# Kernel tuning notes

Measured on AMD Instinct MI355X. Metric: run time of the kernel, lower is better.

The kernel has to match this reference:

```python
import jax, jax.numpy as jnp
import numpy as np

B, S, D = 2, 2048, 1024
H, HD = 16, 64          # n_heads, head_dim (H*HD == D)
E, K, F = 8, 2, 1024    # n_experts, top_k, expert hidden size
EPS = 1e-6


def setup_inputs() -> dict:
    key = jax.random.key(0)
    ks = jax.random.split(key, 10)
    g = lambda k, shape, sc: jax.random.normal(k, shape, jnp.float32) * sc
    return {
        "x": g(ks[0], (B, S, D), 1.0),
        "attn_norm_w": jnp.ones((D,), jnp.float32),
        "wq": g(ks[1], (D, D), 0.02),
        "wk": g(ks[2], (D, D), 0.02),
        "wv": g(ks[3], (D, D), 0.02),
        "wo": g(ks[4], (D, D), 0.02),
        "ffn_norm_w": jnp.ones((D,), jnp.float32),
        "router_w": g(ks[5], (D, E), 0.02),
        "w1": g(ks[6], (E, D, F), 0.02),  # gate proj per expert
        "w3": g(ks[7], (E, D, F), 0.02),  # up proj per expert
        "w2": g(ks[8], (E, F, D), 0.02),  # down proj per expert
    }


def rmsnorm(x, w):
    return x * jax.lax.rsqrt(jnp.mean(x * x, axis=-1, keepdims=True) + EPS) * w


def attention(x, wq, wk, wv, wo):
    b, s, d = x.shape
    q = (x @ wq).reshape(b, s, H, HD)
    k = (x @ wk).reshape(b, s, H, HD)
    v = (x @ wv).reshape(b, s, H, HD)
    scores = jnp.einsum("bqhd,bkhd->bhqk", q, k) / jnp.sqrt(jnp.float32(HD))
    causal = jnp.tril(jnp.ones((s, s), bool))
    scores = jnp.where(causal, scores, jnp.finfo(scores.dtype).min)
    p = jax.nn.softmax(scores, axis=-1)
    o = jnp.einsum("bhqk,bkhd->bqhd", p, v).reshape(b, s, d)
    return o @ wo


def moe_ffn(x, router_w, w1, w2, w3):
    b, s, d = x.shape
    xt = x.reshape(-1, d)                       # [T, D]
    probs = jax.nn.softmax(xt @ router_w, axis=-1)  # [T, E]
    gate, idx = jax.lax.top_k(probs, K)         # [T, K]
    gate = gate / jnp.sum(gate, axis=-1, keepdims=True)  # renormalize top-k
    T = xt.shape[0]
    combine = jnp.zeros((T, E), xt.dtype).at[jnp.arange(T)[:, None], idx].set(gate)
    out = jnp.zeros_like(xt)
    for e in range(E):  # fixed small loop over experts (dense-equivalent dispatch)
        h = jax.nn.silu(xt @ w1[e]) * (xt @ w3[e])
        out = out + combine[:, e:e + 1] * (h @ w2[e])
    return out.reshape(b, s, d)


def reference(x, attn_norm_w, wq, wk, wv, wo, ffn_norm_w, router_w, w1, w2, w3):
    # h = x + dropout(attn(norm(x)));  out = h + dropout(moe(norm(h)))  (dropout=0)
    h = x + attention(rmsnorm(x, attn_norm_w), wq, wk, wv, wo)
    return h + moe_ffn(rmsnorm(h, ffn_norm_w), router_w, w1, w2, w3)
```

## Files before the change

### kernel.cpp

```cpp
#include <hip/hip_runtime.h>
#include <cstdint>
#include <math.h>

typedef unsigned short u16;
typedef unsigned int u32;
typedef __bf16 bf16x8 __attribute__((ext_vector_type(8)));
typedef float f32x4 __attribute__((ext_vector_type(4)));

#define TBATCH 2
#define TSEQ   2048
#define TDIM   1024
#define THEADS 16
#define THDIM  64
#define TEXP   8
#define TFF    1024
#define TTOK   (TBATCH*TSEQ)
#define TPAIRS (TTOK*2)

__device__ __forceinline__ u16 f2bf(float f) {
  u32 u = __float_as_uint(f);
  u += 0x7FFFu + ((u >> 16) & 1u);
  return (u16)(u >> 16);
}
__device__ __forceinline__ u16 f2bft(float f) {
  return (u16)(__float_as_uint(f) >> 16);
}
__device__ __forceinline__ float bf2f(u16 h) { return __uint_as_float(((u32)h) << 16); }
__device__ __forceinline__ float fexp2(float x) {
  float r;
  asm("v_exp_f32 %0, %1" : "=v"(r) : "v"(x));
  return r;
}

__device__ __forceinline__ void gll16(const void* g, void* l) {
  __builtin_amdgcn_global_load_lds((const __attribute__((address_space(1))) void*)g,
                                   (__attribute__((address_space(3))) void*)l, 16, 0, 0);
}
__device__ __forceinline__ bf16x8 ldsread(const void* p) { return *(const bf16x8*)p; }
__device__ __forceinline__ f32x4 mm16(bf16x8 a, bf16x8 b, f32x4 c) {
  return __builtin_amdgcn_mfma_f32_16x16x32_bf16(a, b, c, 0, 0, 0);
}
__device__ __forceinline__ f32x4 fzero() { f32x4 z = {0.f, 0.f, 0.f, 0.f}; return z; }

__global__ void transpose_all_k(const float* __restrict__ wq, const float* __restrict__ wk,
                                const float* __restrict__ wv, const float* __restrict__ wo,
                                const float* __restrict__ w1, const float* __restrict__ w3,
                                const float* __restrict__ w2,
                                u16* __restrict__ qth, u16* __restrict__ qtl,
                                u16* __restrict__ kth, u16* __restrict__ ktl,
                                u16* __restrict__ vth_, u16* __restrict__ vtl_,
                                u16* __restrict__ oth, u16* __restrict__ otl,
                                u16* __restrict__ w1t, u16* __restrict__ w3t, u16* __restrict__ w2t) {
  __shared__ float t[32][33];
  int id = (int)blockIdx.x;
  const float* in; u16* outh; u16* outl = nullptr;
  size_t bo = 0;
  int tile;
  if (id < 4096) {
    const int wi = id >> 10;
    in   = (wi == 0) ? wq  : (wi == 1) ? wk  : (wi == 2) ? wv   : wo;
    outh = (wi == 0) ? qth : (wi == 1) ? kth : (wi == 2) ? vth_ : oth;
    outl = (wi == 0) ? qtl : (wi == 1) ? ktl : (wi == 2) ? vtl_ : otl;
    tile = id & 1023;
  } else {
    const int id2 = id - 4096;
    const int wi = id2 >> 13;
    const int rem = id2 & 8191;
    bo = (size_t)(rem >> 10) << 20;
    in   = (wi == 0) ? w1  : (wi == 1) ? w3  : w2;
    outh = (wi == 0) ? w1t : (wi == 1) ? w3t : w2t;
    tile = rem & 1023;
  }
  const int c0 = (tile & 31) * 32, r0 = (tile >> 5) * 32;
  const int tx = threadIdx.x, ty = threadIdx.y;
#pragma unroll
  for (int j = 0; j < 32; j += 8)
    t[ty + j][tx] = in[bo + (size_t)(r0 + ty + j) * 1024 + (c0 + tx)];
  __syncthreads();
#pragma unroll
  for (int j = 0; j < 32; j += 8) {
    float v = t[tx][ty + j];
    u16 hv = f2bf(v);
    size_t o = bo + (size_t)(c0 + ty + j) * 1024 + (r0 + tx);
    outh[o] = hv;
    if (outl != nullptr) outl[o] = f2bf(v - bf2f(hv));
  }
}

__launch_bounds__(256)
__global__ void rmsnorm_k(const float* __restrict__ x, const float* __restrict__ w,
                          u16* __restrict__ oh, u16* __restrict__ ol) {
  const int t = blockIdx.x, tid = threadIdx.x;
  const float4 xv = ((const float4*)(x + (size_t)t * TDIM))[tid];
  float ss = xv.x*xv.x + xv.y*xv.y + xv.z*xv.z + xv.w*xv.w;
#pragma unroll
  for (int d = 1; d < 64; d <<= 1) ss += __shfl_xor(ss, d, 64);
  __shared__ float sp[4];
  if ((tid & 63) == 0) sp[tid >> 6] = ss;
  __syncthreads();
  const float rsc = rsqrtf((sp[0] + sp[1] + sp[2] + sp[3]) * (1.0f / TDIM) + 1e-6f);
  const float4 wv = ((const float4*)w)[tid];
  float v0 = xv.x*rsc*wv.x, v1 = xv.y*rsc*wv.y, v2 = xv.z*rsc*wv.z, v3 = xv.w*rsc*wv.w;
  u16 h0 = f2bf(v0), h1 = f2bf(v1), h2 = f2bf(v2), h3 = f2bf(v3);
  uint2 ph; ph.x = (u32)h0 | ((u32)h1 << 16); ph.y = (u32)h2 | ((u32)h3 << 16);
  *(uint2*)(oh + (size_t)t * TDIM + tid * 4) = ph;
  u16 l0 = f2bf(v0 - bf2f(h0)), l1 = f2bf(v1 - bf2f(h1));
  u16 l2 = f2bf(v2 - bf2f(h2)), l3 = f2bf(v3 - bf2f(h3));
  uint2 pl; pl.x = (u32)l0 | ((u32)l1 << 16); pl.y = (u32)l2 | ((u32)l3 << 16);
  *(uint2*)(ol + (size_t)t * TDIM + tid * 4) = pl;
}

__launch_bounds__(256)
__global__ void gemm_qkv_k(const u16* __restrict__ Ah, const u16* __restrict__ Al,
                           const u16* __restrict__ Bqh, const u16* __restrict__ Bql,
                           const u16* __restrict__ Bkh, const u16* __restrict__ Bkl,
                           const u16* __restrict__ Bvh, const u16* __restrict__ Bvl,
                           u16* __restrict__ qh, u16* __restrict__ ql,
                           u16* __restrict__ kh, u16* __restrict__ kl,
                           u16* __restrict__ vth, u16* __restrict__ vtl) {
  __shared__ u16 sAh[2][128 * 32], sAl[2][128 * 32], sBh[2][64 * 32], sBl[2][64 * 32];
  const int tid = threadIdx.x, wid = tid >> 6, lane = tid & 63;
  const int which = blockIdx.y >> 4;
  const int m0 = blockIdx.x * 128, n0 = (blockIdx.y & 15) * 64;
  const int wr = wid >> 1, wc = wid & 1;
  const u16* Bth = (which == 0) ? Bqh : (which == 1) ? Bkh : Bvh;
  const u16* Btl = (which == 0) ? Bql : (which == 1) ? Bkl : Bvl;
  u16* outh = (which == 0) ? qh : kh;
  u16* outl = (which == 0) ? ql : kl;

  f32x4 acc[4][2];
#pragma unroll
  for (int i = 0; i < 4; i++)
#pragma unroll
    for (int j = 0; j < 2; j++) acc[i][j] = fzero();

  const int srow = tid >> 2;
  const int scol = (((tid & 3) ^ ((tid >> 3) & 3)) * 8);
  const size_t a0 = (size_t)(m0 + srow) * TDIM + scol;
  const size_t a1 = (size_t)(m0 + srow + 64) * TDIM + scol;
  const size_t b0 = (size_t)(n0 + srow) * TDIM + scol;
  const int ldsw = wid * 1024;

  const int g = (lane >> 1) & 3;
  int aoffs[4], boffs[2];
#pragma unroll
  for (int mf = 0; mf < 4; mf++)
    aoffs[mf] = (wr*64 + mf*16 + (lane & 15)) * 64 + ((((lane >> 4)) ^ g) << 4);
#pragma unroll
  for (int nf = 0; nf < 2; nf++)
    boffs[nf] = (wc*32 + nf*16 + (lane & 15)) * 64 + ((((lane >> 4)) ^ g) << 4);

  auto stage = [&](int kk, int bi) {
    const int ke = kk * 32;
    gll16(Ah + a0 + ke, (char*)sAh[bi] + ldsw);
    gll16(Ah + a1 + ke, (char*)sAh[bi] + 4096 + ldsw);
    gll16(Al + a0 + ke, (char*)sAl[bi] + ldsw);
    gll16(Al + a1 + ke, (char*)sAl[bi] + 4096 + ldsw);
    gll16(Bth + b0 + ke, (char*)sBh[bi] + ldsw);
    gll16(Btl + b0 + ke, (char*)sBl[bi] + ldsw);
  };

  stage(0, 0);
  asm volatile("s_waitcnt vmcnt(0)" ::: "memory");
  __builtin_amdgcn_s_barrier();

  for (int kk = 0; kk < 32; ++kk) {
    const int cur = kk & 1;
    if (kk + 1 < 32) stage(kk + 1, cur ^ 1);
    bf16x8 fah[4], fal[4], fbh[2], fbl[2];
#pragma unroll
    for (int mf = 0; mf < 4; mf++) { fah[mf] = ldsread((char*)sAh[cur] + aoffs[mf]); fal[mf] = ldsread((char*)sAl[cur] + aoffs[mf]); }
#pragma unroll
    for (int nf = 0; nf < 2; nf++) { fbh[nf] = ldsread((char*)sBh[cur] + boffs[nf]); fbl[nf] = ldsread((char*)sBl[cur] + boffs[nf]); }
#pragma unroll
    for (int mf = 0; mf < 4; mf++)
#pragma unroll
      for (int nf = 0; nf < 2; nf++) {
        acc[mf][nf] = mm16(fah[mf], fbh[nf], acc[mf][nf]);
        acc[mf][nf] = mm16(fah[mf], fbl[nf], acc[mf][nf]);
        acc[mf][nf] = mm16(fal[mf], fbh[nf], acc[mf][nf]);
      }
    asm volatile("s_waitcnt vmcnt(0)" ::: "memory");
    __builtin_amdgcn_s_barrier();
  }

#pragma unroll
  for (int mf = 0; mf < 4; mf++)
#pragma unroll
    for (int nf = 0; nf < 2; nf++)
#pragma unroll
      for (int r = 0; r < 4; r++) {
        const int grow = m0 + wr*64 + mf*16 + ((lane >> 4) * 4) + r;
        const int gcol = n0 + wc*32 + nf*16 + (lane & 15);
        const float v = acc[mf][nf][r];
        u16 hv = f2bf(v);
        u16 lv = f2bf(v - bf2f(hv));
        if (which < 2) {
          const size_t o = (size_t)grow * TDIM + gcol;
          outh[o] = hv; outl[o] = lv;
        } else {
          const int b = grow >> 11, s = grow & (TSEQ - 1);
          const int hh = gcol >> 6, hd = gcol & 63;
          const size_t o = ((size_t)((b * THEADS + hh) * THDIM + hd)) * TSEQ + s;
          vth[o] = hv; vtl[o] = lv;
        }
      }
}

template<int EPI>
__launch_bounds__(256)
__global__ void gemm_x3_k(const u16* __restrict__ Ah, const u16* __restrict__ Al,
                          const u16* __restrict__ Bth, const u16* __restrict__ Btl,
                          u16* __restrict__ outh, u16* __restrict__ outl,
                          float* __restrict__ outf, const float* __restrict__ resid,
                          int M, int N, int K) {
  __shared__ u16 sAh[2][128 * 32], sAl[2][128 * 32], sBh[2][64 * 32], sBl[2][64 * 32];
  const int tid = threadIdx.x, wid = tid >> 6, lane = tid & 63;
  const int m0 = blockIdx.x * 128, n0 = blockIdx.y * 64;
  const int wr = wid >> 1, wc = wid & 1;

  f32x4 acc[4][2];
#pragma unroll
  for (int i = 0; i < 4; i++)
#pragma unroll
    for (int j = 0; j < 2; j++) acc[i][j] = fzero();

  const int srow = tid >> 2;
  const int scol = (((tid & 3) ^ ((tid >> 3) & 3)) * 8);
  const size_t a0 = (size_t)(m0 + srow) * K + scol;
  const size_t a1 = (size_t)(m0 + srow + 64) * K + scol;
  const size_t b0 = (size_t)(n0 + srow) * K + scol;
  const int ldsw = wid * 1024;

  const int g = (lane >> 1) & 3;
  int aoffs[4], boffs[2];
#pragma unroll
  for (int mf = 0; mf < 4; mf++)
    aoffs[mf] = (wr*64 + mf*16 + (lane & 15)) * 64 + ((((lane >> 4)) ^ g) << 4);
#pragma unroll
  for (int nf = 0; nf < 2; nf++)
    boffs[nf] = (wc*32 + nf*16 + (lane & 15)) * 64 + ((((lane >> 4)) ^ g) << 4);

  auto stage = [&](int kk, int bi) {
    const int ke = kk * 32;
    gll16(Ah + a0 + ke, (char*)sAh[bi] + ldsw);
    gll16(Ah + a1 + ke, (char*)sAh[bi] + 4096 + ldsw);
    gll16(Al + a0 + ke, (char*)sAl[bi] + ldsw);
    gll16(Al + a1 + ke, (char*)sAl[bi] + 4096 + ldsw);
    gll16(Bth + b0 + ke, (char*)sBh[bi] + ldsw);
    gll16(Btl + b0 + ke, (char*)sBl[bi] + ldsw);
  };

  const int nk = K >> 5;
  stage(0, 0);
  asm volatile("s_waitcnt vmcnt(0)" ::: "memory");
  __builtin_amdgcn_s_barrier();

  for (int kk = 0; kk < nk; ++kk) {
    const int cur = kk & 1;
    if (kk + 1 < nk) stage(kk + 1, cur ^ 1);
    bf16x8 fah[4], fal[4], fbh[2], fbl[2];
#pragma unroll
    for (int mf = 0; mf < 4; mf++) { fah[mf] = ldsread((char*)sAh[cur] + aoffs[mf]); fal[mf] = ldsread((char*)sAl[cur] + aoffs[mf]); }
#pragma unroll
    for (int nf = 0; nf < 2; nf++) { fbh[nf] = ldsread((char*)sBh[cur] + boffs[nf]); fbl[nf] = ldsread((char*)sBl[cur] + boffs[nf]); }
#pragma unroll
    for (int mf = 0; mf < 4; mf++)
#pragma unroll
      for (int nf = 0; nf < 2; nf++) {
        acc[mf][nf] = mm16(fah[mf], fbh[nf], acc[mf][nf]);
        acc[mf][nf] = mm16(fah[mf], fbl[nf], acc[mf][nf]);
        acc[mf][nf] = mm16(fal[mf], fbh[nf], acc[mf][nf]);
      }
    asm volatile("s_waitcnt vmcnt(0)" ::: "memory");
    __builtin_amdgcn_s_barrier();
  }

#pragma unroll
  for (int mf = 0; mf < 4; mf++)
#pragma unroll
    for (int nf = 0; nf < 2; nf++)
#pragma unroll
      for (int r = 0; r < 4; r++) {
        const int grow = m0 + wr*64 + mf*16 + ((lane >> 4) * 4) + r;
        const int gcol = n0 + wc*32 + nf*16 + (lane & 15);
        const float v = acc[mf][nf][r];
        if (EPI == 0) {
          const size_t o = (size_t)grow * N + gcol;
          u16 hv = f2bf(v);
          outh[o] = hv; outl[o] = f2bf(v - bf2f(hv));
        } else if (EPI == 1) {
          const int b = grow >> 11, s = grow & (TSEQ - 1);
          const int hh = gcol >> 6, hd = gcol & 63;
          const size_t o = ((size_t)((b * THEADS + hh) * THDIM + hd)) * TSEQ + s;
          u16 hv = f2bf(v);
          outh[o] = hv; outl[o] = f2bf(v - bf2f(hv));
        } else {
          const size_t o = (size_t)grow * N + gcol;
          outf[o] = v + resid[o];
        }
      }
}

__launch_bounds__(256, 3)
__global__ void flash_k(const u16* __restrict__ Qh, const u16* __restrict__ Ql,
                        const u16* __restrict__ Kh, const u16* __restrict__ Kl,
                        const u16* __restrict__ Vth, const u16* __restrict__ Vtl,
                        u16* __restrict__ Oh, u16* __restrict__ Ol) {
  __shared__ u16 sK[2][2][2048];
  __shared__ u16 sV[2][2][2048];
  __shared__ u16 sP[2][4][512];
  const int tid = threadIdx.x, wid = tid >> 6, lane = tid & 63;
  const int qb = (int)(gridDim.x - 1 - blockIdx.x);
  const int bh = blockIdx.y;
  const int b = bh >> 4, h = bh & 15;
  const float SCL = 0.125f * 1.4426950408889634f;

  bf16x8 fqh[2][2], fql[2][2];
#pragma unroll
  for (int hh = 0; hh < 2; hh++) {
    const size_t qbase = ((size_t)(b * TSEQ + qb * 128 + hh * 64 + wid * 16 + (lane & 15))) * TDIM + h * 64;
#pragma unroll
    for (int kq = 0; kq < 2; kq++) {
      fqh[hh][kq] = *(const bf16x8*)(Qh + qbase + (kq * 4 + (lane >> 4)) * 8);
      fql[hh][kq] = *(const bf16x8*)(Ql + qbase + (kq * 4 + (lane >> 4)) * 8);
    }
  }

  f32x4 oacc[2][4];
  float m_run[2][4], l_lane[2][4];
#pragma unroll
  for (int hh = 0; hh < 2; hh++)
#pragma unroll
    for (int i = 0; i < 4; i++) { oacc[hh][i] = fzero(); m_run[hh][i] = -INFINITY; l_lane[hh][i] = 0.f; }

  const int ksrow = tid >> 3;
  const int ksxcol = (((lane & 7) ^ ((lane >> 3) & 7)) << 3);
  const size_t kg0 = ((size_t)(b * TSEQ + ksrow)) * TDIM + h * 64 + ksxcol;
  const int vsrow = tid >> 2;
  const int vsxcol = (((tid & 3) ^ ((tid >> 3) & 3)) << 3);
  const size_t vg0 = ((size_t)((b * THEADS + h) * THDIM + vsrow)) * TSEQ + vsxcol;

  auto stage = [&](int kb, int bi) {
    const size_t ko = (size_t)kb * 32 * TDIM;
    const size_t vo = (size_t)kb * 32;
    const int wofs = wid * 1024;
    gll16(Kh + kg0 + ko, (char*)sK[bi][0] + wofs);
    gll16(Kl + kg0 + ko, (char*)sK[bi][1] + wofs);
    gll16(Vth + vg0 + vo, (char*)sV[bi][0] + wofs);
    gll16(Vtl + vg0 + vo, (char*)sV[bi][1] + wofs);
  };

  const int nkb = 4 * qb + 4;
  stage(0, 0);
  asm volatile("s_waitcnt vmcnt(0)" ::: "memory");
  __builtin_amdgcn_s_barrier();

  for (int kb = 0; kb < nkb; ++kb) {
    const int cur = kb & 1;
    if (kb + 1 < nkb) stage(kb + 1, cur ^ 1);

    const bool act0 = (kb * 32 <= qb * 128 + 63);

    f32x4 sc[2][2];
#pragma unroll
    for (int nf = 0; nf < 2; nf++) {
      f32x4 s0 = fzero(), s1 = fzero();
      const int krow = nf * 16 + (lane & 15);
#pragma unroll
      for (int kq = 0; kq < 2; kq++) {
        const int off = krow * 128 + (((kq * 4 + (lane >> 4)) ^ (lane & 7)) << 4);
        bf16x8 kfh = ldsread((char*)sK[cur][0] + off);
        bf16x8 kfl = ldsread((char*)sK[cur][1] + off);
        s0 = mm16(fqh[0][kq], kfh, s0);
        s0 = mm16(fqh[0][kq], kfl, s0);
        s0 = mm16(fql[0][kq], kfh, s0);
        s1 = mm16(fqh[1][kq], kfh, s1);
        s1 = mm16(fqh[1][kq], kfl, s1);
        s1 = mm16(fql[1][kq], kfh, s1);
      }
      sc[0][nf] = s0; sc[1][nf] = s1;
    }

    bf16x8 pa_h[2], pa_l[2];
#pragma unroll
    for (int hh = 0; hh < 2; hh++) {
      if (hh == 0 && !act0) continue;

      const int qg = qb * 128 + hh * 64 + wid * 16 + ((lane >> 4) * 4);
      float pm[4] = {-INFINITY, -INFINITY, -INFINITY, -INFINITY};
#pragma unroll
      for (int nf = 0; nf < 2; nf++) {
        const int kg = kb * 32 + nf * 16 + (lane & 15);
#pragma unroll
        for (int r = 0; r < 4; r++) {
          float v = sc[hh][nf][r] * SCL;
          if (kg > qg + r) v = -INFINITY;
          sc[hh][nf][r] = v;
          pm[r] = fmaxf(pm[r], v);
        }
      }
#pragma unroll
      for (int r = 0; r < 4; r++)
#pragma unroll
        for (int d = 1; d < 16; d <<= 1) pm[r] = fmaxf(pm[r], __shfl_xor(pm[r], d, 64));

      float mn[4], esc[4];
#pragma unroll
      for (int r = 0; r < 4; r++) {
        mn[r] = fmaxf(m_run[hh][r], pm[r]);
        esc[r] = fexp2(m_run[hh][r] - mn[r]);
        m_run[hh][r] = mn[r];
      }
      float ls[4] = {0.f, 0.f, 0.f, 0.f};
#pragma unroll
      for (int nf = 0; nf < 2; nf++)
#pragma unroll
        for (int r = 0; r < 4; r++) {
          float p = fexp2(sc[hh][nf][r] - mn[r]);
          sc[hh][nf][r] = p;
          ls[r] += p;
        }
#pragma unroll
      for (int r = 0; r < 4; r++) l_lane[hh][r] = l_lane[hh][r] * esc[r] + ls[r];
#pragma unroll
      for (int nf = 0; nf < 4; nf++)
#pragma unroll
        for (int r = 0; r < 4; r++) oacc[hh][nf][r] *= esc[r];

#pragma unroll
      for (int nf = 0; nf < 2; nf++)
#pragma unroll
        for (int r = 0; r < 4; r++) {
          float p = sc[hh][nf][r];
          u16 ph = f2bft(p);
          const int prow = (lane >> 4) * 4 + r;
          const int pbyte = (prow * 64 + (nf * 16 + (lane & 15)) * 2) ^ (((prow >> 1) & 3) << 4);
          *(u16*)((char*)sP[0][wid] + pbyte) = ph;
          *(u16*)((char*)sP[1][wid] + pbyte) = f2bft(p - bf2f(ph));
        }

      {
        const int prow = lane & 15;
        const int poff = (prow * 64 + ((lane >> 4) << 4)) ^ ((((prow >> 1) & 3)) << 4);
        pa_h[hh] = ldsread((char*)sP[0][wid] + poff);
        pa_l[hh] = ldsread((char*)sP[1][wid] + poff);
      }
    }

#pragma unroll
    for (int nf = 0; nf < 4; nf++) {
      const int vrow = nf * 16 + (lane & 15);
      const int voff = vrow * 64 + ((((lane >> 4) ^ ((lane >> 1) & 3)) & 3) << 4);
      bf16x8 vfh = ldsread((char*)sV[cur][0] + voff);
      bf16x8 vfl = ldsread((char*)sV[cur][1] + voff);
      if (act0) {
        oacc[0][nf] = mm16(pa_h[0], vfh, oacc[0][nf]);
        oacc[0][nf] = mm16(pa_h[0], vfl, oacc[0][nf]);
        oacc[0][nf] = mm16(pa_l[0], vfh, oacc[0][nf]);
      }
      oacc[1][nf] = mm16(pa_h[1], vfh, oacc[1][nf]);
      oacc[1][nf] = mm16(pa_h[1], vfl, oacc[1][nf]);
      oacc[1][nf] = mm16(pa_l[1], vfh, oacc[1][nf]);
    }

    asm volatile("s_waitcnt vmcnt(0)" ::: "memory");
    __builtin_amdgcn_s_barrier();
  }

#pragma unroll
  for (int hh = 0; hh < 2; hh++)
#pragma unroll
    for (int r = 0; r < 4; r++) {
      float lt = l_lane[hh][r];
#pragma unroll
      for (int d = 1; d < 16; d <<= 1) lt += __shfl_xor(lt, d, 64);
      const float inv = 1.0f / lt;
      const int t = b * TSEQ + qb * 128 + hh * 64 + wid * 16 + ((lane >> 4) * 4) + r;
#pragma unroll
      for (int nf = 0; nf < 4; nf++) {
        const float v = oacc[hh][nf][r] * inv;
        const size_t o = (size_t)t * TDIM + h * 64 + nf * 16 + (lane & 15);
        u16 hv = f2bft(v);
        Oh[o] = hv; Ol[o] = f2bft(v - bf2f(hv));
      }
    }
}

__launch_bounds__(256)
__global__ void router_k(const float* __restrict__ hres, const float* __restrict__ wn,
                         const float* __restrict__ rw, u16* __restrict__ hn,
                         int* __restrict__ idx01, float* __restrict__ gate01,
                         int* __restrict__ counts) {
  const int t = blockIdx.x, tid = threadIdx.x;
  const float4 xv = ((const float4*)(hres + (size_t)t * TDIM))[tid];
  float ss = xv.x*xv.x + xv.y*xv.y + xv.z*xv.z + xv.w*xv.w;
#pragma unroll
  for (int d = 1; d < 64; d <<= 1) ss += __shfl_xor(ss, d, 64);
  __shared__ float sp[4];
  __shared__ float sacc[4][8];
  if ((tid & 63) == 0) sp[tid >> 6] = ss;
  __syncthreads();
  const float rsc = rsqrtf((sp[0]+sp[1]+sp[2]+sp[3]) * (1.0f / TDIM) + 1e-6f);
  const float4 wv = ((const float4*)wn)[tid];
  const float x0 = xv.x*rsc*wv.x, x1 = xv.y*rsc*wv.y, x2 = xv.z*rsc*wv.z, x3 = xv.w*rsc*wv.w;
  {
    u16 h0 = f2bf(x0), h1 = f2bf(x1), h2 = f2bf(x2), h3 = f2bf(x3);
    uint2 ph; ph.x = (u32)h0 | ((u32)h1 << 16); ph.y = (u32)h2 | ((u32)h3 << 16);
    *(uint2*)(hn + (size_t)t * TDIM + tid * 4) = ph;
  }
  const float* rp = rw + (size_t)(tid * 4) * TEXP;
  float acc[8];
#pragma unroll
  for (int e = 0; e < 8; e++) acc[e] = x0*rp[e] + x1*rp[8+e] + x2*rp[16+e] + x3*rp[24+e];
#pragma unroll
  for (int e = 0; e < 8; e++)
#pragma unroll
    for (int d = 1; d < 64; d <<= 1) acc[e] += __shfl_xor(acc[e], d, 64);
  if ((tid & 63) == 0)
#pragma unroll
    for (int e = 0; e < 8; e++) sacc[tid >> 6][e] = acc[e];
  __syncthreads();
  if (tid == 0) {
    float lg[8];
#pragma unroll
    for (int e = 0; e < 8; e++) lg[e] = sacc[0][e] + sacc[1][e] + sacc[2][e] + sacc[3][e];
    int i1 = 0;
#pragma unroll
    for (int e = 1; e < 8; e++) if (lg[e] > lg[i1]) i1 = e;
    int i2 = (i1 == 0) ? 1 : 0;
#pragma unroll
    for (int e = 0; e < 8; e++) if (e != i1 && lg[e] > lg[i2]) i2 = e;
    const float g1 = 1.0f / (1.0f + __expf(lg[i2] - lg[i1]));
    idx01[t*2] = i1; idx01[t*2+1] = i2;
    gate01[t*2] = g1; gate01[t*2+1] = 1.0f - g1;
    atomicAdd(&counts[i1], 1);
    atomicAdd(&counts[i2], 1);
  }
}

__global__ void zero8_k(int* counts) { if (threadIdx.x < TEXP) counts[threadIdx.x] = 0; }

__global__ void offsets_k(const int* __restrict__ counts, int* __restrict__ cursor,
                          int* __restrict__ bm_e, int* __restrict__ bm_s0,
                          int* __restrict__ bm_end, int* __restrict__ n_active) {
  if (threadIdx.x != 0 || blockIdx.x != 0) return;
  int off = 0, nb = 0;
  for (int e = 0; e < TEXP; e++) {
    const int c = counts[e];
    cursor[e] = off;
    const int end = off + c;
    for (int mb = 0; mb * 128 < c; mb++) { bm_e[nb] = e; bm_s0[nb] = off + mb * 128; bm_end[nb] = end; nb++; }
    off = end;
  }
  *n_active = nb;
}

__global__ void scatter_k(const int* __restrict__ idx01, int* __restrict__ cursor,
                          int* __restrict__ slot_of, int* __restrict__ perm) {
  const int t = blockIdx.x * 256 + threadIdx.x;
  if (t >= TTOK) return;
#pragma unroll
  for (int k = 0; k < 2; k++) {
    const int e = idx01[t*2+k];
    const int slot = atomicAdd(&cursor[e], 1);
    slot_of[t*2+k] = slot;
    perm[slot] = t;
  }
}

__launch_bounds__(256)
__global__ void moe_gemm1_k(const u16* __restrict__ hn, const u16* __restrict__ w1t,
                            const u16* __restrict__ w3t, const int* __restrict__ perm,
                            const int* __restrict__ bm_e, const int* __restrict__ bm_s0,
                            const int* __restrict__ bm_end, const int* __restrict__ n_active,
                            u16* __restrict__ hbuf) {
  if ((int)blockIdx.x >= *n_active) return;
  __shared__ u16 sA[2][128 * 32], sB1[2][64 * 32], sB3[2][64 * 32];
  const int tid = threadIdx.x, wid = tid >> 6, lane = tid & 63;
  const int e = bm_e[blockIdx.x], slot0 = bm_s0[blockIdx.x], send = bm_end[blockIdx.x];
  const int n0 = blockIdx.y * 64;
  const int wr = wid >> 1, wc = wid & 1;
  const int srow = tid >> 2;
  const int scol = (((tid & 3) ^ ((tid >> 3) & 3)) * 8);
  const int sa0 = slot0 + srow, sa1 = slot0 + srow + 64;
  const int ta = (sa0 < send) ? perm[sa0] : 0;
  const int tb2 = (sa1 < send) ? perm[sa1] : 0;
  const size_t a0 = (size_t)ta * TDIM + scol;
  const size_t a1 = (size_t)tb2 * TDIM + scol;
  const size_t bb = (size_t)e * TDIM * TFF + (size_t)(n0 + srow) * TDIM + scol;
  const int ldsw = wid * 1024;
  f32x4 ac1[4][2], ac3[4][2];
#pragma unroll
  for (int i = 0; i < 4; i++)
#pragma unroll
    for (int j = 0; j < 2; j++) { ac1[i][j] = fzero(); ac3[i][j] = fzero(); }
  const int g = (lane >> 1) & 3;
  int aoffs[4], boffs[2];
#pragma unroll
  for (int mf = 0; mf < 4; mf++)
    aoffs[mf] = (wr*64 + mf*16 + (lane & 15)) * 64 + ((((lane >> 4)) ^ g) << 4);
#pragma unroll
  for (int nf = 0; nf < 2; nf++)
    boffs[nf] = (wc*32 + nf*16 + (lane & 15)) * 64 + ((((lane >> 4)) ^ g) << 4);

  auto stage = [&](int kk, int bi) {
    const int ke = kk * 32;
    gll16(hn + a0 + ke, (char*)sA[bi] + ldsw);
    gll16(hn + a1 + ke, (char*)sA[bi] + 4096 + ldsw);
    gll16(w1t + bb + ke, (char*)sB1[bi] + ldsw);
    gll16(w3t + bb + ke, (char*)sB3[bi] + ldsw);
  };

  stage(0, 0);
  asm volatile("s_waitcnt vmcnt(0)" ::: "memory");
  __builtin_amdgcn_s_barrier();

  for (int kk = 0; kk < 32; ++kk) {
    const int cur = kk & 1;
    if (kk + 1 < 32) stage(kk + 1, cur ^ 1);
    bf16x8 fa[4], f1[2], f3[2];
#pragma unroll
    for (int mf = 0; mf < 4; mf++) fa[mf] = ldsread((char*)sA[cur] + aoffs[mf]);
#pragma unroll
    for (int nf = 0; nf < 2; nf++) { f1[nf] = ldsread((char*)sB1[cur] + boffs[nf]); f3[nf] = ldsread((char*)sB3[cur] + boffs[nf]); }
#pragma unroll
    for (int mf = 0; mf < 4; mf++)
#pragma unroll
      for (int nf = 0; nf < 2; nf++) {
        ac1[mf][nf] = mm16(fa[mf], f1[nf], ac1[mf][nf]);
        ac3[mf][nf] = mm16(fa[mf], f3[nf], ac3[mf][nf]);
      }
    asm volatile("s_waitcnt vmcnt(0)" ::: "memory");
    __builtin_amdgcn_s_barrier();
  }

#pragma unroll
  for (int mf = 0; mf < 4; mf++)
#pragma unroll
    for (int nf = 0; nf < 2; nf++)
#pragma unroll
      for (int r = 0; r < 4; r++) {
        const int slot = slot0 + wr*64 + mf*16 + ((lane >> 4) * 4) + r;
        if (slot < send) {
          const int col = n0 + wc*32 + nf*16 + (lane & 15);
          const float z1 = ac1[mf][nf][r], z3 = ac3[mf][nf][r];
          const float hv = z1 / (1.0f + __expf(-z1)) * z3;
          hbuf[(size_t)slot * TFF + col] = f2bf(hv);
        }
      }
}

__launch_bounds__(256)
__global__ void moe_gemm2_k(const u16* __restrict__ hbuf, const u16* __restrict__ w2t,
                            const int* __restrict__ bm_e, const int* __restrict__ bm_s0,
                            const int* __restrict__ bm_end, const int* __restrict__ n_active,
                            u16* __restrict__ pout) {
  if ((int)blockIdx.x >= *n_active) return;
  __shared__ u16 sA[2][128 * 32], sB[2][64 * 32];
  const int tid = threadIdx.x, wid = tid >> 6, lane = tid & 63;
  const int e = bm_e[blockIdx.x], slot0 = bm_s0[blockIdx.x], send = bm_end[blockIdx.x];
  const int n0 = blockIdx.y * 64;
  const int wr = wid >> 1, wc = wid & 1;
  const int srow = tid >> 2;
  const int scol = (((tid & 3) ^ ((tid >> 3) & 3)) * 8);
  int sa0 = slot0 + srow; if (sa0 > TPAIRS - 1) sa0 = TPAIRS - 1;
  int sa1 = slot0 + srow + 64; if (sa1 > TPAIRS - 1) sa1 = TPAIRS - 1;
  const size_t a0 = (size_t)sa0 * TFF + scol;
  const size_t a1 = (size_t)sa1 * TFF + scol;
  const size_t bb = (size_t)e * TDIM * TFF + (size_t)(n0 + srow) * TFF + scol;
  const int ldsw = wid * 1024;
  f32x4 acc[4][2];
#pragma unroll
  for (int i = 0; i < 4; i++)
#pragma unroll
    for (int j = 0; j < 2; j++) acc[i][j] = fzero();
  const int g = (lane >> 1) & 3;
  int aoffs[4], boffs[2];
#pragma unroll
  for (int mf = 0; mf < 4; mf++)
    aoffs[mf] = (wr*64 + mf*16 + (lane & 15)) * 64 + ((((lane >> 4)) ^ g) << 4);
#pragma unroll
  for (int nf = 0; nf < 2; nf++)
    boffs[nf] = (wc*32 + nf*16 + (lane & 15)) * 64 + ((((lane >> 4)) ^ g) << 4);

  auto stage = [&](int kk, int bi) {
    const int ke = kk * 32;
    gll16(hbuf + a0 + ke, (char*)sA[bi] + ldsw);
    gll16(hbuf + a1 + ke, (char*)sA[bi] + 4096 + ldsw);
    gll16(w2t + bb + ke, (char*)sB[bi] + ldsw);
  };

  stage(0, 0);
  asm volatile("s_waitcnt vmcnt(0)" ::: "memory");
  __builtin_amdgcn_s_barrier();

  for (int kk = 0; kk < 32; ++kk) {
    const int cur = kk & 1;
    if (kk + 1 < 32) stage(kk + 1, cur ^ 1);
    bf16x8 fa[4], fb[2];
#pragma unroll
    for (int mf = 0; mf < 4; mf++) fa[mf] = ldsread((char*)sA[cur] + aoffs[mf]);
#pragma unroll
    for (int nf = 0; nf < 2; nf++) fb[nf] = ldsread((char*)sB[cur] + boffs[nf]);
#pragma unroll
    for (int mf = 0; mf < 4; mf++)
#pragma unroll
      for (int nf = 0; nf < 2; nf++)
        acc[mf][nf] = mm16(fa[mf], fb[nf], acc[mf][nf]);
    asm volatile("s_waitcnt vmcnt(0)" ::: "memory");
    __builtin_amdgcn_s_barrier();
  }

#pragma unroll
  for (int mf = 0; mf < 4; mf++)
#pragma unroll
    for (int nf = 0; nf < 2; nf++)
#pragma unroll
      for (int r = 0; r < 4; r++) {
        const int slot = slot0 + wr*64 + mf*16 + ((lane >> 4) * 4) + r;
        if (slot < send) {
          const int col = n0 + wc*32 + nf*16 + (lane & 15);
          pout[(size_t)slot * TDIM + col] = f2bf(acc[mf][nf][r]);
        }
      }
}

__launch_bounds__(256)
__global__ void combine_k(const float* __restrict__ hres, const u16* __restrict__ pout,
                          const int* __restrict__ slot_of, const float* __restrict__ gate01,
                          float* __restrict__ out) {
  const int t = blockIdx.x, tid = threadIdx.x;
  const int s0 = slot_of[t*2], s1 = slot_of[t*2+1];
  const float g0 = gate01[t*2], g1 = gate01[t*2+1];
  const float4 hv = ((const float4*)(hres + (size_t)t * TDIM))[tid];
  const uint2 u0 = *(const uint2*)(pout + (size_t)s0 * TDIM + tid * 4);
  const uint2 u1 = *(const uint2*)(pout + (size_t)s1 * TDIM + tid * 4);
  float4 o;
  o.x = hv.x + g0 * bf2f((u16)(u0.x & 0xffff)) + g1 * bf2f((u16)(u1.x & 0xffff));
  o.y = hv.y + g0 * bf2f((u16)(u0.x >> 16))    + g1 * bf2f((u16)(u1.x >> 16));
  o.z = hv.z + g0 * bf2f((u16)(u0.y & 0xffff)) + g1 * bf2f((u16)(u1.y & 0xffff));
  o.w = hv.w + g0 * bf2f((u16)(u0.y >> 16))    + g1 * bf2f((u16)(u1.y >> 16));
  ((float4*)(out + (size_t)t * TDIM))[tid] = o;
}

extern "C" void kernel_launch(void* const* d_in, const int* in_sizes, int n_in,
                              void* d_out, int out_size, void* d_ws, size_t ws_size,
                              hipStream_t stream) {
  (void)in_sizes; (void)n_in; (void)out_size; (void)ws_size;
  const float* x   = (const float*)d_in[0];
  const float* anw = (const float*)d_in[1];
  const float* wq  = (const float*)d_in[2];
  const float* wk  = (const float*)d_in[3];
  const float* wv  = (const float*)d_in[4];
  const float* wo  = (const float*)d_in[5];
  const float* fnw = (const float*)d_in[6];
  const float* rw  = (const float*)d_in[7];
  const float* w1  = (const float*)d_in[8];
  const float* w3  = (const float*)d_in[9];
  const float* w2  = (const float*)d_in[10];
  float* out = (float*)d_out;

  char* ws = (char*)d_ws;
  size_t off = 0;
  auto take = [&](size_t bytes) -> char* {
    char* p = ws + off;
    off += (bytes + 255) & ~(size_t)255;
    return p;
  };
  const size_t SZ_W = (size_t)TDIM * TDIM * sizeof(u16);
  const size_t SZ_T = (size_t)TTOK * TDIM * sizeof(u16);
  u16* wqt_h = (u16*)take(SZ_W); u16* wqt_l = (u16*)take(SZ_W);
  u16* wkt_h = (u16*)take(SZ_W); u16* wkt_l = (u16*)take(SZ_W);
  u16* wvt_h = (u16*)take(SZ_W); u16* wvt_l = (u16*)take(SZ_W);
  u16* wot_h = (u16*)take(SZ_W); u16* wot_l = (u16*)take(SZ_W);
  u16* w1t = (u16*)take((size_t)TEXP * TDIM * TFF * sizeof(u16));
  u16* w3t = (u16*)take((size_t)TEXP * TDIM * TFF * sizeof(u16));
  u16* w2t = (u16*)take((size_t)TEXP * TDIM * TFF * sizeof(u16));
  u16* xnh = (u16*)take(SZ_T); u16* xnl = (u16*)take(SZ_T);
  u16* qh  = (u16*)take(SZ_T); u16* ql  = (u16*)take(SZ_T);
  u16* kh  = (u16*)take(SZ_T); u16* kl  = (u16*)take(SZ_T);
  u16* vth = (u16*)take(SZ_T); u16* vtl = (u16*)take(SZ_T);
  float* hres = (float*)take((size_t)TTOK * TDIM * sizeof(float));
  int*   idx01  = (int*)take(TTOK * 2 * 4);
  float* gate01 = (float*)take(TTOK * 2 * 4);
  int*   slot_of = (int*)take(TTOK * 2 * 4);
  int*   perm    = (int*)take(TPAIRS * 4);
  int*   counts  = (int*)take(256);
  int*   cursor  = (int*)take(256);
  int*   bm_e    = (int*)take(96 * 4);
  int*   bm_s0   = (int*)take(96 * 4);
  int*   bm_end  = (int*)take(96 * 4);
  int*   n_act   = (int*)take(256);
  u16* oh = xnh; u16* ol = xnl;
  u16* hn = qh;
  u16* hbuf = kh;
  u16* pout = vth;

  transpose_all_k<<<28672, dim3(32, 8), 0, stream>>>(wq, wk, wv, wo, w1, w3, w2,
                                                     wqt_h, wqt_l, wkt_h, wkt_l, wvt_h, wvt_l,
                                                     wot_h, wot_l, w1t, w3t, w2t);
  zero8_k<<<1, 64, 0, stream>>>(counts);
  rmsnorm_k<<<TTOK, 256, 0, stream>>>(x, anw, xnh, xnl);
  gemm_qkv_k<<<dim3(TTOK/128, 48), 256, 0, stream>>>(xnh, xnl, wqt_h, wqt_l, wkt_h, wkt_l,
                                                     wvt_h, wvt_l, qh, ql, kh, kl, vth, vtl);
  flash_k<<<dim3(TSEQ/128, TBATCH*THEADS), 256, 0, stream>>>(qh, ql, kh, kl, vth, vtl, oh, ol);
  gemm_x3_k<2><<<dim3(TTOK/128, TDIM/64), 256, 0, stream>>>(oh, ol, wot_h, wot_l, nullptr, nullptr, hres, x, TTOK, TDIM, TDIM);
  router_k<<<TTOK, 256, 0, stream>>>(hres, fnw, rw, hn, idx01, gate01, counts);
  offsets_k<<<1, 1, 0, stream>>>(counts, cursor, bm_e, bm_s0, bm_end, n_act);
  scatter_k<<<TTOK/256, 256, 0, stream>>>(idx01, cursor, slot_of, perm);
  moe_gemm1_k<<<dim3(72, TFF/64), 256, 0, stream>>>(hn, w1t, w3t, perm, bm_e, bm_s0, bm_end, n_act, hbuf);
  moe_gemm2_k<<<dim3(72, TDIM/64), 256, 0, stream>>>(hbuf, w2t, bm_e, bm_s0, bm_end, n_act, pout);
  combine_k<<<TTOK, 256, 0, stream>>>(hres, pout, slot_of, gate01, out);
}
```

Baseline: 615.4 us.

## Split flash attention KV range across two blocks with lazy rescaling and combine

```diff
diff --git a/kernel.cpp b/kernel.cpp
--- a/kernel.cpp
+++ b/kernel.cpp
@@ -184,6 +184,7 @@
     __builtin_amdgcn_s_barrier();
   }
 
+  const float qscale = (which == 0) ? 0.18033688011112042f : 1.0f;
 #pragma unroll
   for (int mf = 0; mf < 4; mf++)
 #pragma unroll
@@ -192,7 +193,7 @@
       for (int r = 0; r < 4; r++) {
         const int grow = m0 + wr*64 + mf*16 + ((lane >> 4) * 4) + r;
         const int gcol = n0 + wc*32 + nf*16 + (lane & 15);
-        const float v = acc[mf][nf][r];
+        const float v = acc[mf][nf][r] * qscale;
         u16 hv = f2bf(v);
         u16 lv = f2bf(v - bf2f(hv));
         if (which < 2) {
@@ -302,11 +303,10 @@
       }
 }
 
-__launch_bounds__(256, 3)
 __global__ void flash_k(const u16* __restrict__ Qh, const u16* __restrict__ Ql,
                         const u16* __restrict__ Kh, const u16* __restrict__ Kl,
                         const u16* __restrict__ Vth, const u16* __restrict__ Vtl,
-                        u16* __restrict__ Oh, u16* __restrict__ Ol) {
+                        float* __restrict__ Op, float* __restrict__ ml) {
   __shared__ u16 sK[2][2][2048];
   __shared__ u16 sV[2][2][2048];
   __shared__ u16 sP[2][4][512];
@@ -314,7 +314,7 @@
   const int qb = (int)(gridDim.x - 1 - blockIdx.x);
   const int bh = blockIdx.y;
   const int b = bh >> 4, h = bh & 15;
-  const float SCL = 0.125f * 1.4426950408889634f;
+  const int sp = blockIdx.z;
 
   bf16x8 fqh[2][2], fql[2][2];
 #pragma unroll
@@ -351,18 +351,20 @@
     gll16(Vtl + vg0 + vo, (char*)sV[bi][1] + wofs);
   };
 
-  const int nkb = 4 * qb + 4;
-  stage(0, 0);
+  const int nhalf = 2 * qb + 2;
+  const int kb0 = sp * nhalf, kb1 = kb0 + nhalf;
+  stage(kb0, 0);
   asm volatile("s_waitcnt vmcnt(0)" ::: "memory");
   __builtin_amdgcn_s_barrier();
 
-  for (int kb = 0; kb < nkb; ++kb) {
-    const int cur = kb & 1;
-    if (kb + 1 < nkb) stage(kb + 1, cur ^ 1);
+  for (int kb = kb0; kb < kb1; ++kb) {
+    const int cur = (kb - kb0) & 1;
+    if (kb + 1 < kb1) stage(kb + 1, cur ^ 1);
 
     const bool act0 = (kb * 32 <= qb * 128 + 63);
 
     f32x4 sc[2][2];
+    __builtin_amdgcn_s_setprio(1);
 #pragma unroll
     for (int nf = 0; nf < 2; nf++) {
       f32x4 s0 = fzero(), s1 = fzero();
@@ -381,6 +383,7 @@
       }
       sc[0][nf] = s0; sc[1][nf] = s1;
     }
+    __builtin_amdgcn_s_setprio(0);
 
     bf16x8 pa_h[2], pa_l[2];
 #pragma unroll
@@ -394,7 +397,7 @@
         const int kg = kb * 32 + nf * 16 + (lane & 15);
 #pragma unroll
         for (int r = 0; r < 4; r++) {
-          float v = sc[hh][nf][r] * SCL;
+          float v = sc[hh][nf][r];
           if (kg > qg + r) v = -INFINITY;
           sc[hh][nf][r] = v;
           pm[r] = fmaxf(pm[r], v);
@@ -405,28 +408,30 @@
 #pragma unroll
         for (int d = 1; d < 16; d <<= 1) pm[r] = fmaxf(pm[r], __shfl_xor(pm[r], d, 64));
 
-      float mn[4], esc[4];
-#pragma unroll
-      for (int r = 0; r < 4; r++) {
-        mn[r] = fmaxf(m_run[hh][r], pm[r]);
-        esc[r] = fexp2(m_run[hh][r] - mn[r]);
-        m_run[hh][r] = mn[r];
+      const float dm = fmaxf(fmaxf(pm[0] - m_run[hh][0], pm[1] - m_run[hh][1]),
+                             fmaxf(pm[2] - m_run[hh][2], pm[3] - m_run[hh][3]));
+      if (!__all(dm <= 8.0f)) {
+#pragma unroll
+        for (int r = 0; r < 4; r++) {
+          const float mn = fmaxf(m_run[hh][r], pm[r]);
+          const float esc = fexp2(m_run[hh][r] - mn);
+          m_run[hh][r] = mn;
+          l_lane[hh][r] *= esc;
+#pragma unroll
+          for (int nf = 0; nf < 4; nf++) oacc[hh][nf][r] *= esc;
+        }
       }
       float ls[4] = {0.f, 0.f, 0.f, 0.f};
 #pragma unroll
       for (int nf = 0; nf < 2; nf++)
 #pragma unroll
         for (int r = 0; r < 4; r++) {
-          float p = fexp2(sc[hh][nf][r] - mn[r]);
+          float p = fexp2(sc[hh][nf][r] - m_run[hh][r]);
           sc[hh][nf][r] = p;
           ls[r] += p;
         }
 #pragma unroll
-      for (int r = 0; r < 4; r++) l_lane[hh][r] = l_lane[hh][r] * esc[r] + ls[r];
-#pragma unroll
-      for (int nf = 0; nf < 4; nf++)
-#pragma unroll
-        for (int r = 0; r < 4; r++) oacc[hh][nf][r] *= esc[r];
+      for (int r = 0; r < 4; r++) l_lane[hh][r] += ls[r];
 
 #pragma unroll
       for (int nf = 0; nf < 2; nf++)
@@ -448,6 +453,7 @@
       }
     }
 
+    __builtin_amdgcn_s_setprio(1);
 #pragma unroll
     for (int nf = 0; nf < 4; nf++) {
       const int vrow = nf * 16 + (lane & 15);
@@ -463,6 +469,7 @@
       oacc[1][nf] = mm16(pa_h[1], vfl, oacc[1][nf]);
       oacc[1][nf] = mm16(pa_l[1], vfh, oacc[1][nf]);
     }
+    __builtin_amdgcn_s_setprio(0);
 
     asm volatile("s_waitcnt vmcnt(0)" ::: "memory");
     __builtin_amdgcn_s_barrier();
@@ -475,16 +482,45 @@
       float lt = l_lane[hh][r];
 #pragma unroll
       for (int d = 1; d < 16; d <<= 1) lt += __shfl_xor(lt, d, 64);
-      const float inv = 1.0f / lt;
       const int t = b * TSEQ + qb * 128 + hh * 64 + wid * 16 + ((lane >> 4) * 4) + r;
-#pragma unroll
-      for (int nf = 0; nf < 4; nf++) {
-        const float v = oacc[hh][nf][r] * inv;
-        const size_t o = (size_t)t * TDIM + h * 64 + nf * 16 + (lane & 15);
-        u16 hv = f2bft(v);
-        Oh[o] = hv; Ol[o] = f2bft(v - bf2f(hv));
+      const size_t ob = ((size_t)sp * TTOK + t) * TDIM + h * 64 + (lane & 15);
+#pragma unroll
+      for (int nf = 0; nf < 4; nf++)
+        Op[ob + nf * 16] = oacc[hh][nf][r];
+      if ((lane & 15) == 0) {
+        const size_t mo = (((size_t)sp * TTOK + t) * THEADS + h) * 2;
+        ml[mo] = m_run[hh][r];
+        ml[mo + 1] = lt;
       }
     }
+}
+
+__launch_bounds__(256)
+__global__ void flash_comb_k(const float* __restrict__ Op, const float* __restrict__ ml,
+                             u16* __restrict__ Oh, u16* __restrict__ Ol) {
+  const int t = blockIdx.x, tid = threadIdx.x;
+  const int h = tid >> 4;
+  const size_t m0o = (((size_t)t) * THEADS + h) * 2;
+  const size_t m1o = (((size_t)TTOK + t) * THEADS + h) * 2;
+  const float m0 = ml[m0o], l0 = ml[m0o + 1];
+  const float m1 = ml[m1o], l1 = ml[m1o + 1];
+  const float M = fmaxf(m0, m1);
+  float w0 = fexp2(m0 - M), w1 = fexp2(m1 - M);
+  const float inv = 1.0f / (w0 * l0 + w1 * l1);
+  w0 *= inv; w1 *= inv;
+  const float4 o0 = ((const float4*)(Op + (size_t)t * TDIM))[tid];
+  const float4 o1 = ((const float4*)(Op + ((size_t)TTOK + t) * TDIM))[tid];
+  const float vx = o0.x * w0 + o1.x * w1;
+  const float vy = o0.y * w0 + o1.y * w1;
+  const float vz = o0.z * w0 + o1.z * w1;
+  const float vw = o0.w * w0 + o1.w * w1;
+  u16 hx = f2bft(vx), hy = f2bft(vy), hz = f2bft(vz), hw = f2bft(vw);
+  uint2 ph; ph.x = (u32)hx | ((u32)hy << 16); ph.y = (u32)hz | ((u32)hw << 16);
+  *(uint2*)(Oh + (size_t)t * TDIM + tid * 4) = ph;
+  u16 lx = f2bft(vx - bf2f(hx)), ly = f2bft(vy - bf2f(hy));
+  u16 lz = f2bft(vz - bf2f(hz)), lw = f2bft(vw - bf2f(hw));
+  uint2 pl; pl.x = (u32)lx | ((u32)ly << 16); pl.y = (u32)lz | ((u32)lw << 16);
+  *(uint2*)(Ol + (size_t)t * TDIM + tid * 4) = pl;
 }
 
 __launch_bounds__(256)
@@ -782,6 +818,8 @@
   u16* kh  = (u16*)take(SZ_T); u16* kl  = (u16*)take(SZ_T);
   u16* vth = (u16*)take(SZ_T); u16* vtl = (u16*)take(SZ_T);
   float* hres = (float*)take((size_t)TTOK * TDIM * sizeof(float));
+  float* opart = (float*)take((size_t)2 * TTOK * TDIM * sizeof(float));
+  float* mlbuf = (float*)take((size_t)2 * TTOK * THEADS * 2 * sizeof(float));
   int*   idx01  = (int*)take(TTOK * 2 * 4);
   float* gate01 = (float*)take(TTOK * 2 * 4);
   int*   slot_of = (int*)take(TTOK * 2 * 4);
@@ -804,7 +842,8 @@
   rmsnorm_k<<<TTOK, 256, 0, stream>>>(x, anw, xnh, xnl);
   gemm_qkv_k<<<dim3(TTOK/128, 48), 256, 0, stream>>>(xnh, xnl, wqt_h, wqt_l, wkt_h, wkt_l,
                                                      wvt_h, wvt_l, qh, ql, kh, kl, vth, vtl);
-  flash_k<<<dim3(TSEQ/128, TBATCH*THEADS), 256, 0, stream>>>(qh, ql, kh, kl, vth, vtl, oh, ol);
+  flash_k<<<dim3(TSEQ/128, TBATCH*THEADS, 2), 256, 0, stream>>>(qh, ql, kh, kl, vth, vtl, opart, mlbuf);
+  flash_comb_k<<<TTOK, 256, 0, stream>>>(opart, mlbuf, oh, ol);
   gemm_x3_k<2><<<dim3(TTOK/128, TDIM/64), 256, 0, stream>>>(oh, ol, wot_h, wot_l, nullptr, nullptr, hres, x, TTOK, TDIM, TDIM);
   router_k<<<TTOK, 256, 0, stream>>>(hres, fnw, rw, hn, idx01, gate01, counts);
   offsets_k<<<1, 1, 0, stream>>>(counts, cursor, bm_e, bm_s0, bm_end, n_act);
```

Measured after the change: 794.4 us. 1.29x slower.
